# Performance work log

Hardware: AMD Instinct MI355X
Metric: run time of the kernel (lower is better)

The kernel has to match this reference:

```python
import jax, jax.numpy as jnp
import numpy as np

LAMBDA_FGW = 0.5
TAU_KL = 0.1
N_OUTER = 5
N_SINKHORN = 10
DIM = 512


def _pdist(a, b):
    # sqrt(clamp(||a-b||^2, 1e-6)) computed via expansion (avoids BxKxMxD temp)
    n2 = ((a * a).sum(-1)[:, :, None] + (b * b).sum(-1)[:, None, :]
          - 2.0 * jnp.einsum('bkd,bmd->bkm', a, b))
    return jnp.sqrt(jnp.clip(n2, 1e-6, None))


def setup_inputs() -> dict:
    key = jax.random.key(0)
    ks = jax.random.split(key, 10)
    B, K, M, D = 256, 128, 128, DIM
    inp = {
        'sq': jax.random.normal(ks[0], (B, K, D), jnp.float32),
        'sr': jax.random.normal(ks[1], (B, M, D), jnp.float32),
        'mask_q': jax.random.uniform(ks[2], (B, K), jnp.float32),
        'mask_r': jax.random.uniform(ks[3], (B, M), jnp.float32),
        'centroids_q': jax.random.normal(ks[4], (B, K, D), jnp.float32),
        'centroids_r': jax.random.normal(ks[5], (B, M, D), jnp.float32),
        'W1': jax.random.normal(ks[6], (D, D), jnp.float32) * 0.02,
        'b1': jnp.zeros((D,), jnp.float32),
        'W2': jax.random.normal(ks[7], (D, D), jnp.float32) * 0.02,
        'b2': jnp.zeros((D,), jnp.float32),
        'log_eps': jnp.asarray(np.log(0.05), jnp.float32),
    }
    return inp


def reference(sq, sr, mask_q, mask_r, centroids_q, centroids_r, W1, b1, W2, b2, log_eps):
    proj = lambda x: jax.nn.relu(x @ W1 + b1) @ W2 + b2
    pq, pr = proj(sq), proj(sr)
    C = _pdist(pq, pr)                      # [B,K,M]
    Sq = _pdist(centroids_q, centroids_q)   # [B,K,K]
    Sr = _pdist(centroids_r, centroids_r)   # [B,M,M]

    mu = mask_q / (mask_q.sum(-1, keepdims=True) + 1e-8)  # [B,K]
    nu = mask_r / (mask_r.sum(-1, keepdims=True) + 1e-8)  # [B,M]
    T = mu[:, :, None] * nu[:, None, :]

    eps = jnp.clip(jnp.exp(log_eps), 0.01, 0.5)
    rho = TAU_KL / (TAU_KL + eps)
    log_mu = jnp.log(jnp.clip(mu, 1e-8, None))
    log_nu = jnp.log(jnp.clip(nu, 1e-8, None))
    Sq2, Sr2 = Sq * Sq, Sr * Sr

    C_fgw = C
    for _ in range(N_OUTER):
        t1 = jnp.einsum('bkl,bl->bk', Sq2, T.sum(2))[:, :, None]
        t2 = jnp.einsum('bm,bmn->bn', T.sum(1), Sr2)[:, None, :]
        L_gw = t1 + t2 - 2.0 * jnp.einsum('bkl,blm->bkm', Sq, jnp.einsum('blm,bmn->bln', T, Sr))
        C_fgw = (1.0 - LAMBDA_FGW) * C + LAMBDA_FGW * L_gw
        log_K = -C_fgw / eps
        log_u = jnp.zeros_like(mu)
        log_v = jnp.zeros_like(nu)
        for _ in range(N_SINKHORN):
            log_u = rho * (log_mu - jax.nn.logsumexp(log_K + log_v[:, None, :], axis=2))
            log_v = rho * (log_nu - jax.nn.logsumexp(log_K + log_u[:, :, None], axis=1))
        T = jnp.exp(log_u[:, :, None] + log_K + log_v[:, None, :])

    cost = (T * C_fgw).sum((-1, -2))
    similarity = jax.nn.sigmoid(-cost)
    return similarity, T, C, cost
```

## Files before the change

### kernel.cpp

```cpp
#include <hip/hip_runtime.h>
#include <math.h>

typedef unsigned short u16;
typedef __attribute__((ext_vector_type(4))) float f32x4;
typedef __attribute__((ext_vector_type(8))) short bf16x8;
typedef __attribute__((ext_vector_type(4))) unsigned short u16x4;
typedef __attribute__((ext_vector_type(8))) unsigned short u16x8;

#define DEVI static __device__ __forceinline__

DEVI float b2f(u16 u){ union{float f; unsigned i;} v; v.i = ((unsigned)u)<<16; return v.f; }
DEVI u16 f2b(float f){ union{float f; unsigned i;} v; v.f=f;
  unsigned r = v.i + 0x7fffu + ((v.i>>16)&1u); return (u16)(r>>16); }

DEVI void gload_lds16(const void* g, void* l){
  __builtin_amdgcn_global_load_lds((const __attribute__((address_space(1))) void*)g,
                                   (__attribute__((address_space(3))) void*)l, 16, 0, 0);
}

DEVI f32x4 vmax4(f32x4 a, f32x4 b){
  f32x4 r; r[0]=fmaxf(a[0],b[0]); r[1]=fmaxf(a[1],b[1]);
  r[2]=fmaxf(a[2],b[2]); r[3]=fmaxf(a[3],b[3]); return r;
}

__global__ void prepw_k(const float* __restrict__ W, u16* __restrict__ Wt){
  int id = blockIdx.x*256 + threadIdx.x;
  int k = id>>9, c = id&511;
  Wt[c*512 + k] = f2b(W[id]);
}

__global__ void cvt_k(const float* __restrict__ src, u16* __restrict__ dst,
                      float* __restrict__ norms, int nrows){
  int gw = (int)((blockIdx.x*blockDim.x + threadIdx.x)>>6);
  int lane = threadIdx.x & 63;
  if (gw >= nrows) return;
  const float* s = src + (size_t)gw*512;
  u16* d = dst + (size_t)gw*512;
  float acc = 0.f;
  #pragma unroll
  for (int q=0;q<2;q++){
    f32x4 v = *(const f32x4*)(s + q*256 + lane*4);
    u16x4 u;
    #pragma unroll
    for (int e=0;e<4;e++){
      u16 b = f2b(v[e]); u[e] = b;
      float fv = b2f(b); acc += fv*fv;
    }
    *(u16x4*)(d + q*256 + lane*4) = u;
  }
  #pragma unroll
  for (int off=1;off<64;off<<=1) acc += __shfl_xor(acc, off);
  if (norms != nullptr && lane==0) norms[gw] = acc;
}

__global__ void normb_k(const u16* __restrict__ src, float* __restrict__ norms, int nrows){
  int gw = (int)((blockIdx.x*blockDim.x + threadIdx.x)>>6);
  int lane = threadIdx.x & 63;
  if (gw >= nrows) return;
  const u16* s = src + (size_t)gw*512;
  u16x8 v = *(const u16x8*)(s + lane*8);
  float acc = 0.f;
  #pragma unroll
  for (int e=0;e<8;e++){ float f = b2f(v[e]); acc += f*f; }
  #pragma unroll
  for (int off=1;off<64;off<<=1) acc += __shfl_xor(acc, off);
  if (lane==0) norms[gw] = acc;
}

template<int ACT>
__global__ __launch_bounds__(256) void gemm_k(const u16* __restrict__ X,
    const u16* __restrict__ Wt, const float* __restrict__ bias, u16* __restrict__ OUT){
  __shared__ __align__(16) u16 sA[128*64];
  __shared__ __align__(16) u16 sB[128*64];
  const int tid = threadIdx.x, wave = tid>>6, lane = tid&63;
  const int bid = (blockIdx.x&7)*256 + (blockIdx.x>>3);
  const int rblk = bid>>2, cb = (bid&3)<<7;
  const u16* Xb = X + (size_t)rblk*(128*512);
  const u16* Wb = Wt + (size_t)cb*512;
  const int lrow = lane&15, lg = lane>>4, wr = wave>>1, wc = wave&1;
  f32x4 acc[4][4] = {};
  for (int s=0;s<8;s++){
    const int k0 = s<<6;
    #pragma unroll
    for (int q=0;q<4;q++){
      const int i = (wave<<2)+q;
      const int row = (i<<3) + (lane>>3);
      const int cd = (lane&7) ^ (row&7);
      gload_lds16(Xb + row*512 + k0 + (cd<<3), sA + i*512);
      gload_lds16(Wb + row*512 + k0 + (cd<<3), sB + i*512);
    }
    __syncthreads();
    #pragma unroll
    for (int kh=0;kh<2;kh++){
      bf16x8 a_[4], b_[4];
      #pragma unroll
      for (int i=0;i<4;i++){
        const int ra = (wr<<6)+(i<<4)+lrow;
        a_[i] = *(const bf16x8*)(sA + ra*64 + ((((kh<<2)+lg)^(ra&7))<<3));
        const int rb = (wc<<6)+(i<<4)+lrow;
        b_[i] = *(const bf16x8*)(sB + rb*64 + ((((kh<<2)+lg)^(rb&7))<<3));
      }
      #pragma unroll
      for (int i=0;i<4;i++)
        #pragma unroll
        for (int j=0;j<4;j++)
          acc[i][j] = __builtin_amdgcn_mfma_f32_16x16x32_bf16(a_[i], b_[j], acc[i][j], 0,0,0);
    }
    __syncthreads();
  }
  #pragma unroll
  for (int j=0;j<4;j++){
    const int col = cb + (wc<<6) + (j<<4) + lrow;
    const float bv = bias[col];
    #pragma unroll
    for (int i=0;i<4;i++){
      const int row0 = (rblk<<7) + (wr<<6) + (i<<4) + (lg<<2);
      #pragma unroll
      for (int r=0;r<4;r++){
        float v = acc[i][j][r] + bv;
        if (ACT) v = fmaxf(v, 0.f);
        OUT[(size_t)(row0+r)*512 + col] = f2b(v);
      }
    }
  }
}

template<int MODE>
__global__ __launch_bounds__(256) void pdist_k(const u16* __restrict__ Xa,
    const u16* __restrict__ Xb2, const float* __restrict__ na, const float* __restrict__ nb,
    float* __restrict__ OUT, float* __restrict__ S2t, char* __restrict__ SHL){
  __shared__ __align__(16) u16 sA[128*64];
  __shared__ __align__(16) u16 sB[128*64];
  const int tid = threadIdx.x, wave = tid>>6, lane = tid&63;
  const int b = blockIdx.x;
  const u16* Ab = Xa + (size_t)b*(128*512);
  const u16* Bb = Xb2 + (size_t)b*(128*512);
  const int lrow = lane&15, lg = lane>>4, wr = wave>>1, wc = wave&1;
  f32x4 acc[4][4] = {};
  for (int s=0;s<8;s++){
    const int k0 = s<<6;
    #pragma unroll
    for (int q=0;q<4;q++){
      const int i = (wave<<2)+q;
      const int row = (i<<3) + (lane>>3);
      const int cd = (lane&7) ^ (row&7);
      gload_lds16(Ab + row*512 + k0 + (cd<<3), sA + i*512);
      gload_lds16(Bb + row*512 + k0 + (cd<<3), sB + i*512);
    }
    __syncthreads();
    #pragma unroll
    for (int kh=0;kh<2;kh++){
      bf16x8 a_[4], b_[4];
      #pragma unroll
      for (int i=0;i<4;i++){
        const int ra = (wr<<6)+(i<<4)+lrow;
        a_[i] = *(const bf16x8*)(sA + ra*64 + ((((kh<<2)+lg)^(ra&7))<<3));
        const int rb = (wc<<6)+(i<<4)+lrow;
        b_[i] = *(const bf16x8*)(sB + rb*64 + ((((kh<<2)+lg)^(rb&7))<<3));
      }
      #pragma unroll
      for (int i=0;i<4;i++)
        #pragma unroll
        for (int j=0;j<4;j++)
          acc[i][j] = __builtin_amdgcn_mfma_f32_16x16x32_bf16(a_[i], b_[j], acc[i][j], 0,0,0);
    }
    __syncthreads();
  }
  #pragma unroll
  for (int j=0;j<4;j++){
    const int col = (wc<<6)+(j<<4)+lrow;
    const float nbv = nb[b*128+col];
    #pragma unroll
    for (int i=0;i<4;i++){
      const int row0 = (wr<<6)+(i<<4)+(lg<<2);
      float sv[4];
      #pragma unroll
      for (int r=0;r<4;r++){
        float n2 = na[b*128+row0+r] + nbv - 2.0f*acc[i][j][r];
        sv[r] = sqrtf(fmaxf(n2, 1e-6f));
      }
      if (MODE==0){
        #pragma unroll
        for (int r=0;r<4;r++)
          OUT[(size_t)b*16384 + (size_t)(row0+r)*128 + col] = sv[r];
      } else {
        u16x4 hi4, lo4; f32x4 s2q;
        #pragma unroll
        for (int r=0;r<4;r++){
          u16 h = f2b(sv[r]); hi4[r] = h;
          lo4[r] = f2b(sv[r] - b2f(h));
          s2q[r] = sv[r]*sv[r];
        }
        const int sa = col*256 + ((((row0>>3)^col)&15)<<4) + ((row0&7)<<1);
        char* base = SHL + (size_t)b*65536;
        *(u16x4*)(base + sa) = hi4;
        *(u16x4*)(base + 32768 + sa) = lo4;
        *(f32x4*)(S2t + (size_t)b*16384 + col*128 + row0) = s2q;
      }
    }
  }
}

__global__ void prep_k(const float* __restrict__ mask_q, const float* __restrict__ mask_r,
                       float* __restrict__ lmu, float* __restrict__ lnu,
                       float* __restrict__ mu, float* __restrict__ nu){
  int b = blockIdx.x, t = threadIdx.x;
  __shared__ float red[4];
  float mq = mask_q[b*128+t], mr = mask_r[b*128+t];
  float s1 = mq, s2 = mr;
  #pragma unroll
  for (int off=1;off<64;off<<=1){ s1 += __shfl_xor(s1,off); s2 += __shfl_xor(s2,off); }
  if ((t&63)==0){ red[t>>6] = s1; red[2+(t>>6)] = s2; }
  __syncthreads();
  float sumq = red[0]+red[1], sumr = red[2]+red[3];
  float muv = mq/(sumq+1e-8f), nuv = mr/(sumr+1e-8f);
  lmu[b*128+t] = __logf(fmaxf(muv,1e-8f));
  lnu[b*128+t] = __logf(fmaxf(nuv,1e-8f));
  mu[b*128+t] = muv;
  nu[b*128+t] = nuv;
}

__global__ __launch_bounds__(512,1) void fgw_loop_k(
    const char* __restrict__ SQHL, const char* __restrict__ SRHL,
    const float* __restrict__ SQ2, const float* __restrict__ SR2,
    const float* __restrict__ C_g,
    const float* __restrict__ MU, const float* __restrict__ NU,
    const float* __restrict__ LMU, const float* __restrict__ LNU,
    const float* __restrict__ log_eps,
    float* __restrict__ T_out, float* __restrict__ cost_out, float* __restrict__ sim_out)
{
  __shared__ __align__(16) char bufT[65536];
  __shared__ __align__(16) char bufS[65536];
  __shared__ __align__(16) float avs[128], bvs[128], t1s[128], t2s[128];
  __shared__ __align__(16) float lus[128], lvs[128];
  __shared__ float redc[8];

  const int b = blockIdx.x, tid = threadIdx.x;
  const int w = tid>>6, lane = tid&63, l15 = lane&15, lg = lane>>4;
  const char* SqHLb = SQHL + (size_t)b*65536;
  const char* SrHLb = SRHL + (size_t)b*65536;
  const float* Sq2b = SQ2 + (size_t)b*16384;
  const float* Sr2b = SR2 + (size_t)b*16384;
  const float* Cb   = C_g + (size_t)b*16384;
  const float* MUb  = MU + b*128;
  const float* NUb  = NU + b*128;

  float eps = __expf(log_eps[0]); eps = fminf(fmaxf(eps,0.01f),0.5f);
  const float rho = 0.1f/(0.1f+eps), inve = 1.0f/eps;

  const int kR = 16*w + l15;
  const int nC = kR;
  const int n0 = 16*w + 4*lg;
  const float lmuR = LMU[b*128+kR];
  const float lnuC = LNU[b*128+nC];
  const float muR  = MUb[kR];
  const float nuC  = NUb[nC];

  const int rowA256 = (16*w + l15)*256;
  const int glo2 = lg ^ (l15 & 3);
  const int ghi2 = l15 & 12;
  const int wtail = l15*256 + ((((2*w + (lg>>1)) ^ l15)&15)<<4) + ((lg&1)<<3);

  f32x4 lkR[8], lkC[8];
  float luR = 0.f, lvC = 0.f;

  for (int outer=0; outer<5; outer++){
    #pragma unroll
    for (int r2=0;r2<8;r2++)
      gload_lds16(SrHLb + r2*8192 + tid*16, bufS + r2*8192 + tid*16);
    {
      f32x4 avp = {0.f,0.f,0.f,0.f};
      float bvp = 0.f;
      #pragma unroll
      for (int q=0;q<8;q++){
        f32x4 TRq, TCq;
        if (outer==0){
          const f32x4 nu4 = *(const f32x4*)(NUb + 16*q + 4*lg);
          const f32x4 mu4 = *(const f32x4*)(MUb + 16*q + 4*lg);
          TRq = muR*nu4;
          TCq = mu4*nuC;
        } else {
          const f32x4 lv4 = *(const f32x4*)&lvs[16*q+4*lg];
          const f32x4 lu4 = *(const f32x4*)&lus[16*q+4*lg];
          #pragma unroll
          for (int e=0;e<4;e++){
            TRq[e] = __expf(lkR[q][e] + luR + lv4[e]);
            TCq[e] = __expf(lkC[q][e] + lu4[e] + lvC);
          }
        }
        u16x4 hi4, lo4;
        #pragma unroll
        for (int e=0;e<4;e++){
          u16 h = f2b(TRq[e]); hi4[e] = h;
          lo4[e] = f2b(TRq[e] - b2f(h));
        }
        const int sa = kR*256 + ((((2*q+(lg>>1)) ^ l15)&15)<<4) + ((lg&1)<<3);
        *(u16x4*)(bufT + sa) = hi4;
        *(u16x4*)(bufT + 32768 + sa) = lo4;
        avp += TRq;
        bvp += TCq[0]+TCq[1]+TCq[2]+TCq[3];
      }
      float av = avp[0]+avp[1]+avp[2]+avp[3];
      av += __shfl_xor(av,16); av += __shfl_xor(av,32);
      bvp += __shfl_xor(bvp,16); bvp += __shfl_xor(bvp,32);
      if (lg==0){ avs[kR] = av; bvs[nC] = bvp; }
    }
    __syncthreads();

    {
      const int k = tid>>2, q = tid&3;
      const float* r1 = Sq2b + k*128 + q*32;
      const float* r2p = Sr2b + k*128 + q*32;
      f32x4 a1 = {0.f,0.f,0.f,0.f}, a2 = {0.f,0.f,0.f,0.f};
      #pragma unroll
      for (int i=0;i<8;i++){
        a1 += (*(const f32x4*)(r1+4*i)) * (*(const f32x4*)(avs+q*32+4*i));
        a2 += (*(const f32x4*)(r2p+4*i)) * (*(const f32x4*)(bvs+q*32+4*i));
      }
      float s1 = a1[0]+a1[1]+a1[2]+a1[3];
      float s2 = a2[0]+a2[1]+a2[2]+a2[3];
      s1 += __shfl_xor(s1,1); s1 += __shfl_xor(s1,2);
      s2 += __shfl_xor(s2,1); s2 += __shfl_xor(s2,2);
      if (q==0){ t1s[k]=s1; t2s[k]=s2; }
    }
    f32x4 acc1[8] = {};
    #pragma unroll
    for (int qt=0;qt<4;qt++){
      const int colOff = (((4*qt) ^ ghi2) | glo2) << 4;
      const bf16x8 ahi = *(const bf16x8*)(bufT + rowA256 + colOff);
      const bf16x8 alo = *(const bf16x8*)(bufT + 32768 + rowA256 + colOff);
      const int bbase = l15*256 + colOff;
      #pragma unroll
      for (int nt=0;nt<8;nt++){
        const bf16x8 bhi = *(const bf16x8*)(bufS + nt*4096 + bbase);
        const bf16x8 blo = *(const bf16x8*)(bufS + 32768 + nt*4096 + bbase);
        acc1[nt] = __builtin_amdgcn_mfma_f32_16x16x32_bf16(ahi, bhi, acc1[nt], 0,0,0);
        acc1[nt] = __builtin_amdgcn_mfma_f32_16x16x32_bf16(ahi, blo, acc1[nt], 0,0,0);
        acc1[nt] = __builtin_amdgcn_mfma_f32_16x16x32_bf16(alo, bhi, acc1[nt], 0,0,0);
      }
    }
    __syncthreads();
    #pragma unroll
    for (int r2=0;r2<8;r2++)
      gload_lds16(SqHLb + r2*8192 + tid*16, bufS + r2*8192 + tid*16);
    #pragma unroll
    for (int nt=0;nt<8;nt++){
      u16x4 hi4, lo4;
      #pragma unroll
      for (int r=0;r<4;r++){
        u16 h = f2b(acc1[nt][r]); hi4[r] = h;
        lo4[r] = f2b(acc1[nt][r] - b2f(h));
      }
      const int sa = nt*4096 + wtail;
      *(u16x4*)(bufT + sa) = hi4;
      *(u16x4*)(bufT + 32768 + sa) = lo4;
    }
    __syncthreads();
    f32x4 acc2[8] = {};
    #pragma unroll
    for (int qt=0;qt<4;qt++){
      const int colOff = (((4*qt) ^ ghi2) | glo2) << 4;
      const bf16x8 ahi = *(const bf16x8*)(bufT + rowA256 + colOff);
      const bf16x8 alo = *(const bf16x8*)(bufT + 32768 + rowA256 + colOff);
      const int bbase = l15*256 + colOff;
      #pragma unroll
      for (int kt=0;kt<8;kt++){
        const bf16x8 bhi = *(const bf16x8*)(bufS + kt*4096 + bbase);
        const bf16x8 blo = *(const bf16x8*)(bufS + 32768 + kt*4096 + bbase);
        acc2[kt] = __builtin_amdgcn_mfma_f32_16x16x32_bf16(ahi, bhi, acc2[kt], 0,0,0);
        acc2[kt] = __builtin_amdgcn_mfma_f32_16x16x32_bf16(ahi, blo, acc2[kt], 0,0,0);
        acc2[kt] = __builtin_amdgcn_mfma_f32_16x16x32_bf16(alo, bhi, acc2[kt], 0,0,0);
      }
    }
    f32x4 lkf[8];
    {
      const f32x4 t24 = *(const f32x4*)&t2s[n0];
      #pragma unroll
      for (int kt=0;kt<8;kt++){
        const int k = 16*kt + l15;
        const f32x4 c4 = *(const f32x4*)(Cb + k*128 + n0);
        lkf[kt] = -inve*(0.5f*c4 + 0.5f*(t1s[k] + t24 - 2.0f*acc2[kt]));
      }
    }
    __syncthreads();
    #pragma unroll
    for (int kt=0;kt<8;kt++){
      const int row = 16*kt + l15;
      const int gp = ((4*w+lg) ^ (row&31)) & 31;
      *(f32x4*)(bufT + row*512 + gp*16) = lkf[kt];
      #pragma unroll
      for (int e=0;e<4;e++){
        const int n = n0 + e;
        const int gt = ((4*kt + (l15>>2)) ^ (n&31)) & 31;
        *(float*)(bufS + n*512 + gt*16 + (l15&3)*4) = lkf[kt][e];
      }
    }
    __syncthreads();
    #pragma unroll
    for (int q=0;q<8;q++){
      const int g1 = ((4*q+lg) ^ (kR&31)) & 31;
      lkR[q] = *(const f32x4*)(bufT + kR*512 + g1*16);
      const int g2 = ((4*q+lg) ^ (nC&31)) & 31;
      lkC[q] = *(const f32x4*)(bufS + nC*512 + g2*16);
    }
    for (int it=0; it<10; it++){
      f32x4 y[8];
      #pragma unroll
      for (int q=0;q<8;q++){
        if (it==0) y[q] = lkR[q];
        else       y[q] = lkR[q] + *(const f32x4*)&lvs[16*q+4*lg];
      }
      f32x4 m4 = y[0];
      #pragma unroll
      for (int q=1;q<8;q++) m4 = vmax4(m4, y[q]);
      float mx = fmaxf(fmaxf(m4[0],m4[1]), fmaxf(m4[2],m4[3]));
      mx = fmaxf(mx, __shfl_xor(mx,16));
      mx = fmaxf(mx, __shfl_xor(mx,32));
      f32x4 s4 = {0.f,0.f,0.f,0.f};
      #pragma unroll
      for (int q=0;q<8;q++){
        #pragma unroll
        for (int e=0;e<4;e++) s4[e] += __expf(y[q][e]-mx);
      }
      float s = s4[0]+s4[1]+s4[2]+s4[3];
      s += __shfl_xor(s,16); s += __shfl_xor(s,32);
      luR = rho*(lmuR - (mx + __logf(s)));
      if (lg==0) lus[kR] = luR;
      __syncthreads();
      #pragma unroll
      for (int q=0;q<8;q++)
        y[q] = lkC[q] + *(const f32x4*)&lus[16*q+4*lg];
      m4 = y[0];
      #pragma unroll
      for (int q=1;q<8;q++) m4 = vmax4(m4, y[q]);
      mx = fmaxf(fmaxf(m4[0],m4[1]), fmaxf(m4[2],m4[3]));
      mx = fmaxf(mx, __shfl_xor(mx,16));
      mx = fmaxf(mx, __shfl_xor(mx,32));
      s4 = (f32x4){0.f,0.f,0.f,0.f};
      #pragma unroll
      for (int q=0;q<8;q++){
        #pragma unroll
        for (int e=0;e<4;e++) s4[e] += __expf(y[q][e]-mx);
      }
      s = s4[0]+s4[1]+s4[2]+s4[3];
      s += __shfl_xor(s,16); s += __shfl_xor(s,32);
      lvC = rho*(lnuC - (mx + __logf(s)));
      if (lg==0) lvs[nC] = lvC;
      __syncthreads();
    }
    if (outer==4){
      float cp = 0.f;
      float* Tb = T_out + (size_t)b*16384;
      #pragma unroll
      for (int q=0;q<8;q++){
        const f32x4 lv4 = *(const f32x4*)&lvs[16*q+4*lg];
        f32x4 t;
        #pragma unroll
        for (int e=0;e<4;e++) t[e] = __expf(lkR[q][e] + luR + lv4[e]);
        *(f32x4*)(Tb + kR*128 + 16*q + 4*lg) = t;
        const f32x4 p = t*lkR[q];
        cp += p[0]+p[1]+p[2]+p[3];
      }
      cp *= -eps;
      #pragma unroll
      for (int off=1;off<64;off<<=1) cp += __shfl_xor(cp, off);
      if (lane==0) redc[w] = cp;
      __syncthreads();
      if (tid==0){
        float tot = 0.f;
        #pragma unroll
        for (int w2=0;w2<8;w2++) tot += redc[w2];
        cost_out[b] = tot;
        sim_out[b]  = 1.0f/(1.0f + __expf(tot));
      }
    }
  }
}

extern "C" void kernel_launch(void* const* d_in, const int* in_sizes, int n_in,
                              void* d_out, int out_size, void* d_ws, size_t ws_size,
                              hipStream_t stream){
  const float* sq      = (const float*)d_in[0];
  const float* sr      = (const float*)d_in[1];
  const float* mask_q  = (const float*)d_in[2];
  const float* mask_r  = (const float*)d_in[3];
  const float* cq      = (const float*)d_in[4];
  const float* cr      = (const float*)d_in[5];
  const float* W1      = (const float*)d_in[6];
  const float* b1      = (const float*)d_in[7];
  const float* W2      = (const float*)d_in[8];
  const float* b2      = (const float*)d_in[9];
  const float* log_eps = (const float*)d_in[10];

  float* out  = (float*)d_out;
  float* sim  = out;
  float* Tm   = out + 256;
  float* Cm   = Tm + 4194304;
  float* cost = Cm + 4194304;

  char* ws = (char*)d_ws;
  size_t off = 0;
  auto alloc = [&](size_t bytes)->void*{ void* p = ws + off; off += (bytes+255)&~(size_t)255; return p; };
  u16*   SQB = (u16*)  alloc(33554432);
  u16*   SRB = (u16*)  alloc(33554432);
  u16*   HQ  = (u16*)  alloc(33554432);
  u16*   HR  = (u16*)  alloc(33554432);
  u16*   W1T = (u16*)  alloc(524288);
  u16*   W2T = (u16*)  alloc(524288);
  float* NP  = (float*)alloc(262144);
  float* NCQ = (float*)alloc(131072);
  float* NCR = (float*)alloc(131072);
  float* LMU = (float*)alloc(131072);
  float* LNU = (float*)alloc(131072);
  float* MUA = (float*)alloc(131072);
  float* NUA = (float*)alloc(131072);
  (void)ws_size; (void)in_sizes; (void)n_in; (void)out_size;

  u16* PQ  = SQB;
  u16* CQB = HQ;
  u16* CRB = HR;

  float* SQ2  = (float*)((char*)SQB);
  float* SR2  = (float*)((char*)SQB + 16777216);
  char*  SQHL = (char*)SQB + 33554432;
  char*  SRHL = (char*)SQB + 50331648;

  prepw_k<<<1024,256,0,stream>>>(W1, W1T);
  prepw_k<<<1024,256,0,stream>>>(W2, W2T);
  cvt_k<<<8192,256,0,stream>>>(sq, SQB, nullptr, 32768);
  cvt_k<<<8192,256,0,stream>>>(sr, SRB, nullptr, 32768);
  gemm_k<1><<<2048,256,0,stream>>>(SQB, W1T, b1, HQ);
  gemm_k<0><<<2048,256,0,stream>>>(HQ, W2T, b2, PQ);
  normb_k<<<16384,256,0,stream>>>(PQ, NP, 65536);
  cvt_k<<<8192,256,0,stream>>>(cq, CQB, NCQ, 32768);
  cvt_k<<<8192,256,0,stream>>>(cr, CRB, NCR, 32768);
  pdist_k<0><<<256,256,0,stream>>>(PQ, PQ + (size_t)32768*512, NP, NP + 32768,
                                   Cm, nullptr, nullptr);
  pdist_k<1><<<256,256,0,stream>>>(CQB, CQB, NCQ, NCQ, nullptr, SQ2, SQHL);
  pdist_k<1><<<256,256,0,stream>>>(CRB, CRB, NCR, NCR, nullptr, SR2, SRHL);
  prep_k<<<256,128,0,stream>>>(mask_q, mask_r, LMU, LNU, MUA, NUA);
  fgw_loop_k<<<256,512,0,stream>>>(SQHL, SRHL, SQ2, SR2, Cm, MUA, NUA, LMU, LNU,
                                   log_eps, Tm, cost, sim);
}
```

Baseline: 477.4 us.

## Fuse row norms into GEMM epilogue, drop squared-distance buffers, use base-2 Sinkhorn

Folds the separate row-norm kernel into the second projection GEMM's epilogue, reducing each row with shuffles and atomicAdd after a memset. It stops materializing the fp32 squared distance matrices and instead rebuilds the squares from the hi/lo bf16 split already staged in LDS inside the FGW loop. The Sinkhorn iterations move to the log2 domain with exp2/log2, and the scaled cost is preloaded into registers once. This saves memory traffic and a launch, at the cost of atomics, extra register pressure, and a slight precision change from recomputing squares from the split bf16 values.

```diff
diff --git a/kernel.cpp b/kernel.cpp
--- a/kernel.cpp
+++ b/kernel.cpp
@@ -48,28 +48,17 @@
     }
     *(u16x4*)(d + q*256 + lane*4) = u;
   }
-  #pragma unroll
-  for (int off=1;off<64;off<<=1) acc += __shfl_xor(acc, off);
-  if (norms != nullptr && lane==0) norms[gw] = acc;
-}
-
-__global__ void normb_k(const u16* __restrict__ src, float* __restrict__ norms, int nrows){
-  int gw = (int)((blockIdx.x*blockDim.x + threadIdx.x)>>6);
-  int lane = threadIdx.x & 63;
-  if (gw >= nrows) return;
-  const u16* s = src + (size_t)gw*512;
-  u16x8 v = *(const u16x8*)(s + lane*8);
-  float acc = 0.f;
-  #pragma unroll
-  for (int e=0;e<8;e++){ float f = b2f(v[e]); acc += f*f; }
-  #pragma unroll
-  for (int off=1;off<64;off<<=1) acc += __shfl_xor(acc, off);
-  if (lane==0) norms[gw] = acc;
-}
-
-template<int ACT>
+  if (norms != nullptr){
+    #pragma unroll
+    for (int off=1;off<64;off<<=1) acc += __shfl_xor(acc, off);
+    if (lane==0) norms[gw] = acc;
+  }
+}
+
+template<int ACT, int NORM>
 __global__ __launch_bounds__(256) void gemm_k(const u16* __restrict__ X,
-    const u16* __restrict__ Wt, const float* __restrict__ bias, u16* __restrict__ OUT){
+    const u16* __restrict__ Wt, const float* __restrict__ bias, u16* __restrict__ OUT,
+    float* __restrict__ NP){
   __shared__ __align__(16) u16 sA[128*64];
   __shared__ __align__(16) u16 sB[128*64];
   const int tid = threadIdx.x, wave = tid>>6, lane = tid&63;
@@ -108,6 +97,13 @@
     }
     __syncthreads();
   }
+  float nacc[4][4];
+  if (NORM){
+    #pragma unroll
+    for (int i=0;i<4;i++)
+      #pragma unroll
+      for (int r=0;r<4;r++) nacc[i][r]=0.f;
+  }
   #pragma unroll
   for (int j=0;j<4;j++){
     const int col = cb + (wc<<6) + (j<<4) + lrow;
@@ -119,16 +115,30 @@
       for (int r=0;r<4;r++){
         float v = acc[i][j][r] + bv;
         if (ACT) v = fmaxf(v, 0.f);
-        OUT[(size_t)(row0+r)*512 + col] = f2b(v);
-      }
-    }
+        u16 pb = f2b(v);
+        OUT[(size_t)(row0+r)*512 + col] = pb;
+        if (NORM){ float fv = b2f(pb); nacc[i][r] += fv*fv; }
+      }
+    }
+  }
+  if (NORM){
+    #pragma unroll
+    for (int i=0;i<4;i++)
+      #pragma unroll
+      for (int r=0;r<4;r++){
+        float v = nacc[i][r];
+        v += __shfl_xor(v,1); v += __shfl_xor(v,2);
+        v += __shfl_xor(v,4); v += __shfl_xor(v,8);
+        if (lrow==0)
+          atomicAdd(NP + (rblk<<7) + (wr<<6) + (i<<4) + (lg<<2) + r, v);
+      }
   }
 }
 
 template<int MODE>
 __global__ __launch_bounds__(256) void pdist_k(const u16* __restrict__ Xa,
     const u16* __restrict__ Xb2, const float* __restrict__ na, const float* __restrict__ nb,
-    float* __restrict__ OUT, float* __restrict__ S2t, char* __restrict__ SHL){
+    float* __restrict__ OUT, char* __restrict__ SHL){
   __shared__ __align__(16) u16 sA[128*64];
   __shared__ __align__(16) u16 sB[128*64];
   const int tid = threadIdx.x, wave = tid>>6, lane = tid&63;
@@ -184,25 +194,23 @@
         for (int r=0;r<4;r++)
           OUT[(size_t)b*16384 + (size_t)(row0+r)*128 + col] = sv[r];
       } else {
-        u16x4 hi4, lo4; f32x4 s2q;
+        u16x4 hi4, lo4;
         #pragma unroll
         for (int r=0;r<4;r++){
           u16 h = f2b(sv[r]); hi4[r] = h;
           lo4[r] = f2b(sv[r] - b2f(h));
-          s2q[r] = sv[r]*sv[r];
         }
         const int sa = col*256 + ((((row0>>3)^col)&15)<<4) + ((row0&7)<<1);
         char* base = SHL + (size_t)b*65536;
         *(u16x4*)(base + sa) = hi4;
         *(u16x4*)(base + 32768 + sa) = lo4;
-        *(f32x4*)(S2t + (size_t)b*16384 + col*128 + row0) = s2q;
       }
     }
   }
 }
 
 __global__ void prep_k(const float* __restrict__ mask_q, const float* __restrict__ mask_r,
-                       float* __restrict__ lmu, float* __restrict__ lnu,
+                       float* __restrict__ lmu2, float* __restrict__ lnu2,
                        float* __restrict__ mu, float* __restrict__ nu){
   int b = blockIdx.x, t = threadIdx.x;
   __shared__ float red[4];
@@ -214,18 +222,17 @@
   __syncthreads();
   float sumq = red[0]+red[1], sumr = red[2]+red[3];
   float muv = mq/(sumq+1e-8f), nuv = mr/(sumr+1e-8f);
-  lmu[b*128+t] = __logf(fmaxf(muv,1e-8f));
-  lnu[b*128+t] = __logf(fmaxf(nuv,1e-8f));
+  lmu2[b*128+t] = __log2f(fmaxf(muv,1e-8f));
+  lnu2[b*128+t] = __log2f(fmaxf(nuv,1e-8f));
   mu[b*128+t] = muv;
   nu[b*128+t] = nuv;
 }
 
 __global__ __launch_bounds__(512,1) void fgw_loop_k(
     const char* __restrict__ SQHL, const char* __restrict__ SRHL,
-    const float* __restrict__ SQ2, const float* __restrict__ SR2,
     const float* __restrict__ C_g,
     const float* __restrict__ MU, const float* __restrict__ NU,
-    const float* __restrict__ LMU, const float* __restrict__ LNU,
+    const float* __restrict__ LMU2, const float* __restrict__ LNU2,
     const float* __restrict__ log_eps,
     float* __restrict__ T_out, float* __restrict__ cost_out, float* __restrict__ sim_out)
 {
@@ -239,27 +246,28 @@
   const int w = tid>>6, lane = tid&63, l15 = lane&15, lg = lane>>4;
   const char* SqHLb = SQHL + (size_t)b*65536;
   const char* SrHLb = SRHL + (size_t)b*65536;
-  const float* Sq2b = SQ2 + (size_t)b*16384;
-  const float* Sr2b = SR2 + (size_t)b*16384;
   const float* Cb   = C_g + (size_t)b*16384;
   const float* MUb  = MU + b*128;
   const float* NUb  = NU + b*128;
 
   float eps = __expf(log_eps[0]); eps = fminf(fmaxf(eps,0.01f),0.5f);
-  const float rho = 0.1f/(0.1f+eps), inve = 1.0f/eps;
+  const float rho = 0.1f/(0.1f+eps);
+  const float hscale = 0.5f*1.4426950408889634f/eps;
 
   const int kR = 16*w + l15;
-  const int nC = kR;
   const int n0 = 16*w + 4*lg;
-  const float lmuR = LMU[b*128+kR];
-  const float lnuC = LNU[b*128+nC];
-  const float muR  = MUb[kR];
-  const float nuC  = NUb[nC];
+  const float lmu2R = LMU2[b*128+kR];
+  const float lnu2C = LNU2[b*128+kR];
 
   const int rowA256 = (16*w + l15)*256;
   const int glo2 = lg ^ (l15 & 3);
   const int ghi2 = l15 & 12;
   const int wtail = l15*256 + ((((2*w + (lg>>1)) ^ l15)&15)<<4) + ((lg&1)<<3);
+
+  f32x4 Cf2[8];
+  #pragma unroll
+  for (int kt=0;kt<8;kt++)
+    Cf2[kt] = -hscale * (*(const f32x4*)(Cb + (size_t)(16*kt+l15)*128 + n0));
 
   f32x4 lkR[8], lkC[8];
   float luR = 0.f, lvC = 0.f;
@@ -273,55 +281,61 @@
       float bvp = 0.f;
       #pragma unroll
       for (int q=0;q<8;q++){
-        f32x4 TRq, TCq;
+        f32x4 TR, TC;
         if (outer==0){
           const f32x4 nu4 = *(const f32x4*)(NUb + 16*q + 4*lg);
           const f32x4 mu4 = *(const f32x4*)(MUb + 16*q + 4*lg);
-          TRq = muR*nu4;
-          TCq = mu4*nuC;
+          const float muR = MUb[kR], nuC = NUb[kR];
+          TR = muR*nu4; TC = mu4*nuC;
         } else {
-          const f32x4 lv4 = *(const f32x4*)&lvs[16*q+4*lg];
-          const f32x4 lu4 = *(const f32x4*)&lus[16*q+4*lg];
+          const f32x4 lv4 = *(const f32x4*)&lvs[16*q + 4*lg];
+          const f32x4 lu4 = *(const f32x4*)&lus[16*q + 4*lg];
           #pragma unroll
           for (int e=0;e<4;e++){
-            TRq[e] = __expf(lkR[q][e] + luR + lv4[e]);
-            TCq[e] = __expf(lkC[q][e] + lu4[e] + lvC);
+            TR[e] = exp2f(lkR[q][e] + luR + lv4[e]);
+            TC[e] = exp2f(lkC[q][e] + lu4[e] + lvC);
           }
         }
         u16x4 hi4, lo4;
         #pragma unroll
         for (int e=0;e<4;e++){
-          u16 h = f2b(TRq[e]); hi4[e] = h;
-          lo4[e] = f2b(TRq[e] - b2f(h));
+          u16 h = f2b(TR[e]); hi4[e] = h;
+          lo4[e] = f2b(TR[e] - b2f(h));
         }
         const int sa = kR*256 + ((((2*q+(lg>>1)) ^ l15)&15)<<4) + ((lg&1)<<3);
         *(u16x4*)(bufT + sa) = hi4;
         *(u16x4*)(bufT + 32768 + sa) = lo4;
-        avp += TRq;
-        bvp += TCq[0]+TCq[1]+TCq[2]+TCq[3];
+        avp += TR;
+        bvp += TC[0]+TC[1]+TC[2]+TC[3];
       }
       float av = avp[0]+avp[1]+avp[2]+avp[3];
       av += __shfl_xor(av,16); av += __shfl_xor(av,32);
       bvp += __shfl_xor(bvp,16); bvp += __shfl_xor(bvp,32);
-      if (lg==0){ avs[kR] = av; bvs[nC] = bvp; }
+      if (lg==0){ avs[kR] = av; bvs[kR] = bvp; }
     }
     __syncthreads();
 
     {
-      const int k = tid>>2, q = tid&3;
-      const float* r1 = Sq2b + k*128 + q*32;
-      const float* r2p = Sr2b + k*128 + q*32;
-      f32x4 a1 = {0.f,0.f,0.f,0.f}, a2 = {0.f,0.f,0.f,0.f};
-      #pragma unroll
-      for (int i=0;i<8;i++){
-        a1 += (*(const f32x4*)(r1+4*i)) * (*(const f32x4*)(avs+q*32+4*i));
-        a2 += (*(const f32x4*)(r2p+4*i)) * (*(const f32x4*)(bvs+q*32+4*i));
-      }
-      float s1 = a1[0]+a1[1]+a1[2]+a1[3];
-      float s2 = a2[0]+a2[1]+a2[2]+a2[3];
-      s1 += __shfl_xor(s1,1); s1 += __shfl_xor(s1,2);
+      const int p = tid>>2, sub = tid&3;
+      float s2 = 0.f;
+      #pragma unroll
+      for (int gg=0; gg<4; gg++){
+        const int g = 4*sub+gg;
+        const int off = p*256 + (((g ^ (p&15))&15)<<4);
+        const u16x8 h8 = *(const u16x8*)(bufS + off);
+        const u16x8 l8 = *(const u16x8*)(bufS + 32768 + off);
+        const f32x4 bva = *(const f32x4*)&bvs[8*g];
+        const f32x4 bvb = *(const f32x4*)&bvs[8*g+4];
+        #pragma unroll
+        for (int e=0;e<4;e++){
+          float x = b2f(h8[e]) + b2f(l8[e]);
+          s2 = fmaf(bva[e], x*x, s2);
+          float y2 = b2f(h8[4+e]) + b2f(l8[4+e]);
+          s2 = fmaf(bvb[e], y2*y2, s2);
+        }
+      }
       s2 += __shfl_xor(s2,1); s2 += __shfl_xor(s2,2);
-      if (q==0){ t1s[k]=s1; t2s[k]=s2; }
+      if (sub==0) t2s[p] = s2;
     }
     f32x4 acc1[8] = {};
     #pragma unroll
@@ -340,6 +354,7 @@
       }
     }
     __syncthreads();
+
     #pragma unroll
     for (int r2=0;r2<8;r2++)
       gload_lds16(SqHLb + r2*8192 + tid*16, bufS + r2*8192 + tid*16);
@@ -356,6 +371,29 @@
       *(u16x4*)(bufT + 32768 + sa) = lo4;
     }
     __syncthreads();
+
+    {
+      const int p = tid>>2, sub = tid&3;
+      float s1 = 0.f;
+      #pragma unroll
+      for (int gg=0; gg<4; gg++){
+        const int g = 4*sub+gg;
+        const int off = p*256 + (((g ^ (p&15))&15)<<4);
+        const u16x8 h8 = *(const u16x8*)(bufS + off);
+        const u16x8 l8 = *(const u16x8*)(bufS + 32768 + off);
+        const f32x4 ava = *(const f32x4*)&avs[8*g];
+        const f32x4 avb = *(const f32x4*)&avs[8*g+4];
+        #pragma unroll
+        for (int e=0;e<4;e++){
+          float x = b2f(h8[e]) + b2f(l8[e]);
+          s1 = fmaf(ava[e], x*x, s1);
+          float y2 = b2f(h8[4+e]) + b2f(l8[4+e]);
+          s1 = fmaf(avb[e], y2*y2, s1);
+        }
+      }
+      s1 += __shfl_xor(s1,1); s1 += __shfl_xor(s1,2);
+      if (sub==0) t1s[p] = s1;
+    }
     f32x4 acc2[8] = {};
     #pragma unroll
     for (int qt=0;qt<4;qt++){
@@ -372,17 +410,17 @@
         acc2[kt] = __builtin_amdgcn_mfma_f32_16x16x32_bf16(alo, bhi, acc2[kt], 0,0,0);
       }
     }
+    __syncthreads();
+
     f32x4 lkf[8];
     {
       const f32x4 t24 = *(const f32x4*)&t2s[n0];
       #pragma unroll
       for (int kt=0;kt<8;kt++){
-        const int k = 16*kt + l15;
-        const f32x4 c4 = *(const f32x4*)(Cb + k*128 + n0);
-        lkf[kt] = -inve*(0.5f*c4 + 0.5f*(t1s[k] + t24 - 2.0f*acc2[kt]));
-      }
-    }
-    __syncthreads();
+        const float t1v = t1s[16*kt+l15];
+        lkf[kt] = Cf2[kt] + hscale*(2.0f*acc2[kt] - t1v - t24);
+      }
+    }
     #pragma unroll
     for (int kt=0;kt<8;kt++){
       const int row = 16*kt + l15;
@@ -400,54 +438,51 @@
     for (int q=0;q<8;q++){
       const int g1 = ((4*q+lg) ^ (kR&31)) & 31;
       lkR[q] = *(const f32x4*)(bufT + kR*512 + g1*16);
-      const int g2 = ((4*q+lg) ^ (nC&31)) & 31;
-      lkC[q] = *(const f32x4*)(bufS + nC*512 + g2*16);
-    }
+      lkC[q] = *(const f32x4*)(bufS + kR*512 + g1*16);
+    }
+
     for (int it=0; it<10; it++){
       f32x4 y[8];
       #pragma unroll
       for (int q=0;q<8;q++){
-        if (it==0) y[q] = lkR[q];
-        else       y[q] = lkR[q] + *(const f32x4*)&lvs[16*q+4*lg];
-      }
-      f32x4 m4 = y[0];
-      #pragma unroll
-      for (int q=1;q<8;q++) m4 = vmax4(m4, y[q]);
+        y[q] = lkR[q];
+        if (it) y[q] += *(const f32x4*)&lvs[16*q+4*lg];
+      }
+      f32x4 m4 = vmax4(vmax4(vmax4(y[0],y[1]),vmax4(y[2],y[3])),
+                       vmax4(vmax4(y[4],y[5]),vmax4(y[6],y[7])));
       float mx = fmaxf(fmaxf(m4[0],m4[1]), fmaxf(m4[2],m4[3]));
-      mx = fmaxf(mx, __shfl_xor(mx,16));
-      mx = fmaxf(mx, __shfl_xor(mx,32));
+      mx = fmaxf(mx,__shfl_xor(mx,16)); mx = fmaxf(mx,__shfl_xor(mx,32));
       f32x4 s4 = {0.f,0.f,0.f,0.f};
       #pragma unroll
       for (int q=0;q<8;q++){
         #pragma unroll
-        for (int e=0;e<4;e++) s4[e] += __expf(y[q][e]-mx);
+        for (int e=0;e<4;e++) s4[e] += exp2f(y[q][e]-mx);
       }
       float s = s4[0]+s4[1]+s4[2]+s4[3];
       s += __shfl_xor(s,16); s += __shfl_xor(s,32);
-      luR = rho*(lmuR - (mx + __logf(s)));
+      luR = rho*(lmu2R - (mx + __log2f(s)));
       if (lg==0) lus[kR] = luR;
       __syncthreads();
       #pragma unroll
       for (int q=0;q<8;q++)
         y[q] = lkC[q] + *(const f32x4*)&lus[16*q+4*lg];
-      m4 = y[0];
-      #pragma unroll
-      for (int q=1;q<8;q++) m4 = vmax4(m4, y[q]);
+      m4 = vmax4(vmax4(vmax4(y[0],y[1]),vmax4(y[2],y[3])),
+                 vmax4(vmax4(y[4],y[5]),vmax4(y[6],y[7])));
       mx = fmaxf(fmaxf(m4[0],m4[1]), fmaxf(m4[2],m4[3]));
-      mx = fmaxf(mx, __shfl_xor(mx,16));
-      mx = fmaxf(mx, __shfl_xor(mx,32));
+      mx = fmaxf(mx,__shfl_xor(mx,16)); mx = fmaxf(mx,__shfl_xor(mx,32));
       s4 = (f32x4){0.f,0.f,0.f,0.f};
       #pragma unroll
       for (int q=0;q<8;q++){
         #pragma unroll
-        for (int e=0;e<4;e++) s4[e] += __expf(y[q][e]-mx);
+        for (int e=0;e<4;e++) s4[e] += exp2f(y[q][e]-mx);
       }
       s = s4[0]+s4[1]+s4[2]+s4[3];
       s += __shfl_xor(s,16); s += __shfl_xor(s,32);
-      lvC = rho*(lnuC - (mx + __logf(s)));
-      if (lg==0) lvs[nC] = lvC;
+      lvC = rho*(lnu2C - (mx + __log2f(s)));
+      if (lg==0) lvs[kR] = lvC;
       __syncthreads();
     }
+
     if (outer==4){
       float cp = 0.f;
       float* Tb = T_out + (size_t)b*16384;
@@ -456,12 +491,12 @@
         const f32x4 lv4 = *(const f32x4*)&lvs[16*q+4*lg];
         f32x4 t;
         #pragma unroll
-        for (int e=0;e<4;e++) t[e] = __expf(lkR[q][e] + luR + lv4[e]);
+        for (int e=0;e<4;e++) t[e] = exp2f(lkR[q][e] + luR + lv4[e]);
         *(f32x4*)(Tb + kR*128 + 16*q + 4*lg) = t;
-        const f32x4 p = t*lkR[q];
-        cp += p[0]+p[1]+p[2]+p[3];
-      }
-      cp *= -eps;
+        const f32x4 pr = t*lkR[q];
+        cp += pr[0]+pr[1]+pr[2]+pr[3];
+      }
+      cp *= -eps*0.6931471805599453f;
       #pragma unroll
       for (int off=1;off<64;off<<=1) cp += __shfl_xor(cp, off);
       if (lane==0) redc[w] = cp;
@@ -520,25 +555,23 @@
   u16* CQB = HQ;
   u16* CRB = HR;
 
-  float* SQ2  = (float*)((char*)SQB);
-  float* SR2  = (float*)((char*)SQB + 16777216);
-  char*  SQHL = (char*)SQB + 33554432;
-  char*  SRHL = (char*)SQB + 50331648;
+  char* SQHL = (char*)SQB;
+  char* SRHL = (char*)SQB + 16777216;
 
   prepw_k<<<1024,256,0,stream>>>(W1, W1T);
   prepw_k<<<1024,256,0,stream>>>(W2, W2T);
   cvt_k<<<8192,256,0,stream>>>(sq, SQB, nullptr, 32768);
   cvt_k<<<8192,256,0,stream>>>(sr, SRB, nullptr, 32768);
-  gemm_k<1><<<2048,256,0,stream>>>(SQB, W1T, b1, HQ);
-  gemm_k<0><<<2048,256,0,stream>>>(HQ, W2T, b2, PQ);
-  normb_k<<<16384,256,0,stream>>>(PQ, NP, 65536);
+  gemm_k<1,0><<<2048,256,0,stream>>>(SQB, W1T, b1, HQ, nullptr);
+  hipMemsetAsync(NP, 0, 262144, stream);
+  gemm_k<0,1><<<2048,256,0,stream>>>(HQ, W2T, b2, PQ, NP);
   cvt_k<<<8192,256,0,stream>>>(cq, CQB, NCQ, 32768);
   cvt_k<<<8192,256,0,stream>>>(cr, CRB, NCR, 32768);
   pdist_k<0><<<256,256,0,stream>>>(PQ, PQ + (size_t)32768*512, NP, NP + 32768,
-                                   Cm, nullptr, nullptr);
-  pdist_k<1><<<256,256,0,stream>>>(CQB, CQB, NCQ, NCQ, nullptr, SQ2, SQHL);
-  pdist_k<1><<<256,256,0,stream>>>(CRB, CRB, NCR, NCR, nullptr, SR2, SRHL);
+                                   Cm, nullptr);
+  pdist_k<1><<<256,256,0,stream>>>(CQB, CQB, NCQ, NCQ, nullptr, SQHL);
+  pdist_k<1><<<256,256,0,stream>>>(CRB, CRB, NCR, NCR, nullptr, SRHL);
   prep_k<<<256,128,0,stream>>>(mask_q, mask_r, LMU, LNU, MUA, NUA);
-  fgw_loop_k<<<256,512,0,stream>>>(SQHL, SRHL, SQ2, SR2, Cm, MUA, NUA, LMU, LNU,
+  fgw_loop_k<<<256,512,0,stream>>>(SQHL, SRHL, Cm, MUA, NUA, LMU, LNU,
                                    log_eps, Tm, cost, sim);
 }
```

Result: no change. 484.3 us (+1.4%).
